# Kernel tuning notes

Measured on AMD Instinct MI355X. Metric: run time of the kernel, lower is better.

Reference implementation:

```python
import jax, jax.numpy as jnp
import numpy as np

D = 512; NH = 8; HD = D // NH; SR = 4; B = 8; HH = 64; WW = 64; N = HH * WW
Q = 200; C2 = D // 2; NH2 = NH // 2
SCALE = HD ** -0.5


def _ln(x, g, b):
    m = jnp.mean(x, -1, keepdims=True)
    v = jnp.mean((x - m) ** 2, -1, keepdims=True)
    return (x - m) * jax.lax.rsqrt(v + 1e-5) * g + b


def _relu6(x):
    return jnp.clip(x, 0.0, 6.0)


def _conv(x, w, b, s):
    y = jax.lax.conv_general_dilated(x, w, (s, s), 'VALID',
                                     dimension_numbers=('NCHW', 'OIHW', 'NCHW'))
    return y + b[None, :, None, None]


def _dwconv(x, w, b):
    y = jax.lax.conv_general_dilated(x, w, (1, 1), ((1, 1), (1, 1)),
                                     dimension_numbers=('NCHW', 'OIHW', 'NCHW'),
                                     feature_group_count=x.shape[1])
    return y + b[None, :, None, None]


def setup_inputs():
    key = jax.random.key(0)
    ks = jax.random.split(key, 16)
    conv4_std = float(np.sqrt(2.0 / (16 * D)))   # fan_out = 4*4*D
    conv2_std = float(np.sqrt(2.0 / (4 * D)))    # fan_out = 2*2*D
    dw_std = float(np.sqrt(2.0 / 9.0))           # fan_out = 3*3*C2/C2
    inp = {
        'query': jax.random.normal(ks[0], (Q, B, D), jnp.float32),
        'key': jax.random.normal(ks[1], (B, N, D), jnp.float32),
        'value': jax.random.normal(ks[2], (B, N, D), jnp.float32),
        'q_w': jax.random.normal(ks[3], (D, D), jnp.float32) * 0.02,
        'sr1_1_w': jax.random.normal(ks[4], (D, D, 4, 4), jnp.float32) * conv4_std,
        'sr1_1_b': jnp.zeros((D,), jnp.float32),
        'n1_1_g': jnp.ones((D,), jnp.float32),
        'n1_1_b': jnp.zeros((D,), jnp.float32),
        'sr1_2_w': jax.random.normal(ks[5], (D, D, 4, 4), jnp.float32) * conv4_std,
        'sr1_2_b': jnp.zeros((D,), jnp.float32),
        'n1_2_g': jnp.ones((D,), jnp.float32),
        'n1_2_b': jnp.zeros((D,), jnp.float32),
        'sr2_1_w': jax.random.normal(ks[6], (D, D, 2, 2), jnp.float32) * conv2_std,
        'sr2_1_b': jnp.zeros((D,), jnp.float32),
        'n2_1_g': jnp.ones((D,), jnp.float32),
        'n2_1_b': jnp.zeros((D,), jnp.float32),
        'sr2_2_w': jax.random.normal(ks[7], (D, D, 2, 2), jnp.float32) * conv2_std,
        'sr2_2_b': jnp.zeros((D,), jnp.float32),
        'n2_2_g': jnp.ones((D,), jnp.float32),
        'n2_2_b': jnp.zeros((D,), jnp.float32),
        'k1_w': jax.random.normal(ks[8], (C2, D), jnp.float32) * 0.02,
        'v1_w': jax.random.normal(ks[9], (C2, D), jnp.float32) * 0.02,
        'k2_w': jax.random.normal(ks[10], (C2, D), jnp.float32) * 0.02,
        'v2_w': jax.random.normal(ks[11], (C2, D), jnp.float32) * 0.02,
        'lc1_w': jax.random.normal(ks[12], (C2, 1, 3, 3), jnp.float32) * dw_std,
        'lc1_b': jnp.zeros((C2,), jnp.float32),
        'lc2_w': jax.random.normal(ks[13], (C2, 1, 3, 3), jnp.float32) * dw_std,
        'lc2_b': jnp.zeros((C2,), jnp.float32),
        'proj_w': jax.random.normal(ks[14], (D, D), jnp.float32) * 0.02,
        'proj_b': jnp.zeros((D,), jnp.float32),
        'H': HH,
        'W': WW,
    }
    return inp


def _forward(query, key, value, q_w,
             sr1_1_w, sr1_1_b, n1_1_g, n1_1_b, sr1_2_w, sr1_2_b, n1_2_g, n1_2_b,
             sr2_1_w, sr2_1_b, n2_1_g, n2_1_b, sr2_2_w, sr2_2_b, n2_2_g, n2_2_b,
             k1_w, v1_w, k2_w, v2_w, lc1_w, lc1_b, lc2_w, lc2_b,
             proj_w, proj_b, H, W):
    Qn, Bn, C = query.shape
    h1, w1 = H // SR, W // SR          # branch-1 reduced grid
    h2, w2 = H * 2 // SR, W * 2 // SR  # branch-2 reduced grid

    # q: note original does a raw reshape (Q,B,C)->(B,Q,nh,hd); replicate exactly
    q = (query @ q_w.T).reshape(Bn, Qn, NH, HD).transpose(0, 2, 1, 3)  # (B,NH,Q,HD)

    key_img = key.transpose(0, 2, 1).reshape(Bn, C, H, W)
    val_img = value.transpose(0, 2, 1).reshape(Bn, C, H, W)

    def reduce_branch(img, cw, cb, g, b, s):
        t = _conv(img, cw, cb, s).reshape(Bn, C, -1).transpose(0, 2, 1)  # (B,L,C)
        return _relu6(_ln(t, g, b))

    key_1 = reduce_branch(key_img, sr1_1_w, sr1_1_b, n1_1_g, n1_1_b, SR)
    val_1 = reduce_branch(val_img, sr1_2_w, sr1_2_b, n1_2_g, n1_2_b, SR)
    key_2 = reduce_branch(key_img, sr2_1_w, sr2_1_b, n2_1_g, n2_1_b, SR // 2)
    val_2 = reduce_branch(val_img, sr2_2_w, sr2_2_b, n2_2_g, n2_2_b, SR // 2)

    def heads(t, w):  # (B,L,C) -> (B,NH2,L,HD)
        return (t @ w.T).reshape(Bn, -1, NH2, HD).transpose(0, 2, 1, 3)

    k1 = heads(key_1, k1_w)
    v1 = heads(val_1, v1_w)
    k2 = heads(key_2, k2_w)
    v2 = heads(val_2, v2_w)

    def branch(qh, kh, vh, lw, lb, hh, ww):
        attn = jax.nn.softmax(jnp.einsum('bhqd,bhkd->bhqk', qh, kh) * SCALE, axis=-1)
        vimg = vh.transpose(0, 2, 1, 3).reshape(Bn, -1, C2).transpose(0, 2, 1)
        vimg = vimg.reshape(Bn, C2, hh, ww)
        vloc = _dwconv(vimg, lw, lb).reshape(Bn, NH2, HD, -1).transpose(0, 1, 3, 2)
        xh = jnp.einsum('bhqk,bhkd->bhqd', attn, vh + vloc)
        # original: .transpose(1,2).reshape(Q,B,C//2) -- raw reshape, replicate
        return xh.transpose(0, 2, 1, 3).reshape(Qn, Bn, C2)

    x1 = branch(q[:, :NH2], k1, v1, lc1_w, lc1_b, h1, w1)
    x2 = branch(q[:, NH2:], k2, v2, lc2_w, lc2_b, h2, w2)
    x = jnp.concatenate([x1, x2], axis=-1)
    return x @ proj_w.T + proj_b


def reference(query, key, value, q_w,
              sr1_1_w, sr1_1_b, n1_1_g, n1_1_b, sr1_2_w, sr1_2_b, n1_2_g, n1_2_b,
              sr2_1_w, sr2_1_b, n2_1_g, n2_1_b, sr2_2_w, sr2_2_b, n2_2_g, n2_2_b,
              k1_w, v1_w, k2_w, v2_w, lc1_w, lc1_b, lc2_w, lc2_b,
              proj_w, proj_b, H, W):
    return _forward(query, key, value, q_w,
                    sr1_1_w, sr1_1_b, n1_1_g, n1_1_b, sr1_2_w, sr1_2_b, n1_2_g, n1_2_b,
                    sr2_1_w, sr2_1_b, n2_1_g, n2_1_b, sr2_2_w, sr2_2_b, n2_2_g, n2_2_b,
                    k1_w, v1_w, k2_w, v2_w, lc1_w, lc1_b, lc2_w, lc2_b,
                    proj_w, proj_b, H, W)
```

## Files before the change

### kernel.cpp

```cpp
#include <hip/hip_runtime.h>
#include <cstddef>

#define QN   200
#define DIM  512
#define NHEAD 8
#define HD   64
#define C2   256
#define NH2  4
#define NTOK 4096

typedef unsigned short ushort_t;
typedef short s16x4 __attribute__((ext_vector_type(4)));
typedef short s16x8 __attribute__((ext_vector_type(8)));
typedef float f32x4 __attribute__((ext_vector_type(4)));

__device__ __forceinline__ unsigned short f2bf(float f) {
    unsigned int u = __float_as_uint(f);
    u += 0x7fffu + ((u >> 16) & 1u);
    return (unsigned short)(u >> 16);
}
__device__ __forceinline__ float bf2f(unsigned short u) {
    return __uint_as_float(((unsigned int)u) << 16);
}
__device__ __forceinline__ s16x8 pack8(float4 x, float4 y) {
    s16x8 v;
    v[0] = (short)f2bf(x.x); v[1] = (short)f2bf(x.y);
    v[2] = (short)f2bf(x.z); v[3] = (short)f2bf(x.w);
    v[4] = (short)f2bf(y.x); v[5] = (short)f2bf(y.y);
    v[6] = (short)f2bf(y.z); v[7] = (short)f2bf(y.w);
    return v;
}

__global__ __launch_bounds__(256) void cvt_f2b(
    const float* __restrict__ src, ushort_t* __restrict__ dst, int n8)
{
    const int i = blockIdx.x * 256 + threadIdx.x;
    if (i >= n8) return;
    const float4 a = ((const float4*)src)[i * 2];
    const float4 b = ((const float4*)src)[i * 2 + 1];
    ((s16x8*)dst)[i] = pack8(a, b);
}

struct CDesc { const float* s; ushort_t* d; };
struct CPack { CDesc c[7]; int bound[7]; };
__global__ __launch_bounds__(256) void prep_kernel(CPack pk)
{
    const int bid = blockIdx.x;
    int idx = 0;
#pragma unroll
    for (int i = 0; i < 6; ++i) idx += (bid >= pk.bound[i]);
    const int base = idx ? pk.bound[idx - 1] : 0;
    const int i = (bid - base) * 256 + threadIdx.x;
    const float4 a = ((const float4*)pk.c[idx].s)[i * 2];
    const float4 b = ((const float4*)pk.c[idx].s)[i * 2 + 1];
    ((s16x8*)pk.c[idx].d)[i] = pack8(a, b);
}

__global__ __launch_bounds__(256) void wtrans_kernel(
    const float* __restrict__ w, ushort_t* __restrict__ wt, int KK, int lKK)
{
    __shared__ float tile[512 * 17];
    const int c = blockIdx.x;
    const int K = KK << 9;
    const float* src = w + (size_t)c * K;
    ushort_t* dst = wt + (size_t)c * K;
    for (int i = threadIdx.x; i < K; i += 256) {
        int ci = i >> lKK, p = i & (KK - 1);
        tile[ci * (KK + 1) + p] = src[i];
    }
    __syncthreads();
    for (int i = threadIdx.x; i < K; i += 256) {
        int p = i >> 9, ci = i & 511;
        dst[i] = f2bf(tile[ci * (KK + 1) + p]);
    }
}

__global__ __launch_bounds__(256) void conv_gemm(
    const ushort_t* __restrict__ Ap, const ushort_t* __restrict__ Bp,
    float* __restrict__ Cp, int M, int N, int K, int klen,
    int lOW, int ls, int lMT)
{
    constexpr int ASZ = 128 * 64;
    constexpr int BSZ = 64 * 64;
    __shared__ short lds[2 * (ASZ + BSZ)];

    const int tid = threadIdx.x;
    const int bid = blockIdx.x;
    const int xcd = bid & 7;
    const int j = bid >> 3;
    const int nt = j & 7;
    const int mz = (j >> 3) * 8 + xcd;
    const int mt = mz & ((1 << lMT) - 1);
    const int z = mz >> lMT;
    const int m0 = mt * 128, n0 = nt * 64;
    const int kstart = z * klen;

    const int lane = tid & 63, wave = tid >> 6;
    const int l16 = lane & 15, quad = lane >> 4;
    const int wm = (wave >> 1) * 64;
    const int wn = (wave & 1) * 32;

    auto off = [](int r, int c) -> int {
        return (r << 6) + ((c ^ (r & 7)) << 3);
    };

    unsigned abase[4]; int offA[4], acx[4];
#pragma unroll
    for (int i = 0; i < 4; ++i) {
        const int g = tid + i * 256;
        const int r = g >> 3, c = g & 7;
        acx[i] = c * 8;
        offA[i] = off(r, c);
        const int OW = 1 << lOW;
        const int m = m0 + r;
        const int bidx = m >> (2 * lOW);
        const int pix = m & (OW * OW - 1);
        const int oy = pix >> lOW, ox = pix & (OW - 1);
        abase[i] = (unsigned)(bidx * NTOK + (oy << ls) * 64 + (ox << ls)) << 9;
    }
    unsigned bbase[2]; int offB[2], bcx[2];
#pragma unroll
    for (int i = 0; i < 2; ++i) {
        const int g = tid + i * 256;
        const int r = g >> 3, c = g & 7;
        bcx[i] = c * 8;
        offB[i] = off(r, c);
        bbase[i] = (unsigned)(n0 + r) * K;
    }

    s16x8 aR[4], bR[2];
    auto loadg = [&](int t) {
        const int k0 = kstart + t * 64;
#pragma unroll
        for (int i = 0; i < 4; ++i) {
            const int k = k0 + acx[i];
            const int p = k >> 9;
            const int ky = p >> ls, kx = p & ((1 << ls) - 1);
            const unsigned o = abase[i] + ((unsigned)(ky * 64 + kx) << 9) + (k & 511);
            aR[i] = *(const s16x8*)(Ap + o);
        }
#pragma unroll
        for (int i = 0; i < 2; ++i)
            bR[i] = *(const s16x8*)(Bp + bbase[i] + k0 + bcx[i]);
    };
    auto stg = [&](int buf) {
        short* A = lds + buf * (ASZ + BSZ);
        short* Bs = A + ASZ;
#pragma unroll
        for (int i = 0; i < 4; ++i) *(s16x8*)&A[offA[i]] = aR[i];
#pragma unroll
        for (int i = 0; i < 2; ++i) *(s16x8*)&Bs[offB[i]] = bR[i];
    };

    f32x4 acc[4][2];
#pragma unroll
    for (int a = 0; a < 4; ++a)
#pragma unroll
        for (int b = 0; b < 2; ++b)
            acc[a][b] = (f32x4){0.f, 0.f, 0.f, 0.f};

    loadg(0);
    stg(0);
    __syncthreads();
    const int nk = klen >> 6;
    for (int t = 0; t < nk; ++t) {
        if (t + 1 < nk) loadg(t + 1);
        const short* A = lds + (t & 1) * (ASZ + BSZ);
        const short* Bs = A + ASZ;
#pragma unroll
        for (int kk = 0; kk < 2; ++kk) {
            s16x8 af[4], bf[2];
#pragma unroll
            for (int f = 0; f < 4; ++f)
                af[f] = *(const s16x8*)&A[off(wm + f * 16 + l16, quad + kk * 4)];
#pragma unroll
            for (int f = 0; f < 2; ++f)
                bf[f] = *(const s16x8*)&Bs[off(wn + f * 16 + l16, quad + kk * 4)];
#pragma unroll
            for (int a = 0; a < 4; ++a)
#pragma unroll
                for (int b = 0; b < 2; ++b)
                    acc[a][b] = __builtin_amdgcn_mfma_f32_16x16x32_bf16(
                        af[a], bf[b], acc[a][b], 0, 0, 0);
        }
        if (t + 1 < nk) {
            stg((t + 1) & 1);
            __syncthreads();
        }
    }

    const unsigned zoff = (unsigned)z * (unsigned)M * (unsigned)N;
#pragma unroll
    for (int a = 0; a < 4; ++a) {
        const int m = m0 + wm + a * 16 + quad * 4;
#pragma unroll
        for (int b = 0; b < 2; ++b) {
            const int n = n0 + wn + b * 16 + l16;
#pragma unroll
            for (int r = 0; r < 4; ++r)
                Cp[zoff + (unsigned)(m + r) * N + n] = acc[a][b][r];
        }
    }
}

template <int OBF>
__device__ __forceinline__ void gemm64_k512(
    short* lds, const ushort_t* __restrict__ Ab, const ushort_t* __restrict__ Bp,
    const float* __restrict__ bias, void* __restrict__ Cp_,
    int m0, int n0, int N, float oscale)
{
    const int tid = threadIdx.x;
    const int lane = tid & 63, wave = tid >> 6;
    const int l16 = lane & 15, quad = lane >> 4;
    const int wm = (wave >> 1) * 32;
    const int wn = (wave & 1) * 32;

    auto off = [](int r, int c) -> int {
        return ((r >> 1) << 6) + (((((r & 1) << 2) | c) ^ ((r >> 1) & 7)) << 3);
    };

    const int cs = (tid & 3) * 8;
    const int ofA = off(tid >> 2, tid & 3);
    const unsigned ab = (unsigned)(m0 + (tid >> 2)) * 512;
    const unsigned bb = (unsigned)(n0 + (tid >> 2)) * 512;

    s16x8 aR, bR;
    auto loadg = [&](int t) {
        aR = *(const s16x8*)(Ab + ab + t * 32 + cs);
        bR = *(const s16x8*)(Bp + bb + t * 32 + cs);
    };
    auto stg = [&](int buf) {
        short* A = lds + buf * 4096;
        short* Bs = A + 2048;
        *(s16x8*)&A[ofA] = aR;
        *(s16x8*)&Bs[ofA] = bR;
    };

    f32x4 acc[2][2];
#pragma unroll
    for (int a = 0; a < 2; ++a)
#pragma unroll
        for (int b = 0; b < 2; ++b)
            acc[a][b] = (f32x4){0.f, 0.f, 0.f, 0.f};

    loadg(0); stg(0); __syncthreads();
#pragma unroll 1
    for (int t = 0; t < 16; ++t) {
        if (t + 1 < 16) loadg(t + 1);
        const short* A = lds + (t & 1) * 4096;
        const short* Bs = A + 2048;
        s16x8 af[2], bfv[2];
#pragma unroll
        for (int f = 0; f < 2; ++f)
            af[f] = *(const s16x8*)&A[off(wm + f * 16 + l16, quad)];
#pragma unroll
        for (int f = 0; f < 2; ++f)
            bfv[f] = *(const s16x8*)&Bs[off(wn + f * 16 + l16, quad)];
#pragma unroll
        for (int a = 0; a < 2; ++a)
#pragma unroll
            for (int b = 0; b < 2; ++b)
                acc[a][b] = __builtin_amdgcn_mfma_f32_16x16x32_bf16(
                    af[a], bfv[b], acc[a][b], 0, 0, 0);
        if (t + 1 < 16) { stg((t + 1) & 1); __syncthreads(); }
    }

#pragma unroll
    for (int a = 0; a < 2; ++a) {
        const int m = m0 + wm + a * 16 + quad * 4;
#pragma unroll
        for (int b = 0; b < 2; ++b) {
            const int n = n0 + wn + b * 16 + l16;
            const float bv = bias ? bias[n] : 0.f;
#pragma unroll
            for (int r = 0; r < 4; ++r) {
                const float val = acc[a][b][r] * oscale + bv;
                if constexpr (OBF)
                    ((ushort_t*)Cp_)[(unsigned)(m + r) * N + n] = f2bf(val);
                else
                    ((float*)Cp_)[(unsigned)(m + r) * N + n] = val;
            }
        }
    }
}

struct PDesc { const ushort_t* A; const ushort_t* B; ushort_t* C; int lnT; float scale; };
struct PPack { PDesc d[5]; int bound[5]; };
__global__ __launch_bounds__(256) void proj_gemm(PPack pk)
{
    __shared__ short lds[8192];
    const int bid = blockIdx.x;
    int idx = 0;
#pragma unroll
    for (int i = 0; i < 4; ++i) idx += (bid >= pk.bound[i]);
    const PDesc d = pk.d[idx];
    const int base = idx ? pk.bound[idx - 1] : 0;
    const int loc = bid - base;
    const int nt = loc & ((1 << d.lnT) - 1);
    const int mt = loc >> d.lnT;
    gemm64_k512<1>(lds, d.A, d.B, nullptr, d.C, mt * 64, nt * 64, 64 << d.lnT, d.scale);
}

__global__ __launch_bounds__(256) void final_gemm(
    const ushort_t* __restrict__ A, const ushort_t* __restrict__ B,
    const float* __restrict__ bias, float* __restrict__ C)
{
    __shared__ short lds[8192];
    const int m0 = (blockIdx.x >> 3) * 64;
    const int n0 = (blockIdx.x & 7) * 64;
    gemm64_k512<0>(lds, A, B, bias, C, m0, n0, 512, 1.0f);
}

__global__ __launch_bounds__(256) void ln_relu6_kernel(
    ushort_t* __restrict__ dst, const float* __restrict__ src, unsigned pstride,
    int np, const float* __restrict__ cb, const float* __restrict__ g,
    const float* __restrict__ bta)
{
    const int row = blockIdx.x * 4 + (threadIdx.x >> 6);
    const int lane = threadIdx.x & 63;
    float v[8];
#pragma unroll
    for (int j = 0; j < 8; ++j) v[j] = cb[lane + 64 * j];
    const float* p = src + (size_t)row * DIM;
    for (int ip = 0; ip < np; ++ip) {
#pragma unroll
        for (int j = 0; j < 8; ++j) v[j] += p[lane + 64 * j];
        p += pstride;
    }
    float s1 = 0.f, s2 = 0.f;
#pragma unroll
    for (int j = 0; j < 8; ++j) { s1 += v[j]; s2 += v[j] * v[j]; }
#pragma unroll
    for (int off = 32; off; off >>= 1) {
        s1 += __shfl_xor(s1, off, 64);
        s2 += __shfl_xor(s2, off, 64);
    }
    const float mean = s1 * (1.0f / DIM);
    const float var = s2 * (1.0f / DIM) - mean * mean;
    const float rstd = rsqrtf(var + 1e-5f);
    ushort_t* q = dst + (size_t)row * DIM;
#pragma unroll
    for (int j = 0; j < 8; ++j) {
        const int c = lane + 64 * j;
        float y = (v[j] - mean) * rstd * g[c] + bta[c];
        q[c] = f2bf(fminf(fmaxf(y, 0.0f), 6.0f));
    }
}

__device__ __forceinline__ void vplus_body(
    const ushort_t* __restrict__ vbuf, const float* __restrict__ lw,
    const float* __restrict__ lb, ushort_t* __restrict__ out,
    int lOW, int lL, int blk)
{
    const int idx = blk * 256 + threadIdx.x;
    const int c = idx & 255;
    const int pix = (idx >> 8) & ((1 << lL) - 1);
    const int b = idx >> (8 + lL);
    const int OW = 1 << lOW;
    const int y = pix >> lOW, x = pix & (OW - 1);
    float acc = lb[c];
#pragma unroll
    for (int dy = -1; dy <= 1; ++dy) {
        const int ny = y + dy;
        if ((unsigned)ny >= (unsigned)OW) continue;
#pragma unroll
        for (int dx = -1; dx <= 1; ++dx) {
            const int nx = x + dx;
            if ((unsigned)nx >= (unsigned)OW) continue;
            acc += bf2f(vbuf[(((unsigned)(b << lL) + ny * OW + nx) << 8) + c]) *
                   lw[c * 9 + (dy + 1) * 3 + (dx + 1)];
        }
    }
    out[idx] = f2bf(bf2f(vbuf[idx]) + acc);
}

__global__ __launch_bounds__(256) void vplus2_kernel(
    const ushort_t* v1, const float* w1, const float* b1, ushort_t* o1,
    const ushort_t* v2, const float* w2, const float* b2, ushort_t* o2)
{
    const int bid = blockIdx.x;
    if (bid < 2048) vplus_body(v1, w1, b1, o1, 4, 8, bid);
    else            vplus_body(v2, w2, b2, o2, 5, 10, bid - 2048);
}

template <int L>
__global__ __launch_bounds__(256) void attn_mfma(
    const ushort_t* __restrict__ qbuf, const ushort_t* __restrict__ kbuf,
    const ushort_t* __restrict__ vbuf, ushort_t* __restrict__ xbuf,
    int hoff, int coff)
{
    constexpr int SP = L + 12;
    constexpr int NV = L / 64;
    __shared__ float S[16][SP];
    __shared__ float invs[16];
    __shared__ alignas(16) short Qs[16][72];
    __shared__ alignas(16) short KV[64][72];

    const int tid = threadIdx.x;
    const int qt = blockIdx.x;
    const int h = blockIdx.y;
    const int b = blockIdx.z;
    const int lane = tid & 63, wave = tid >> 6;
    const int l16 = lane & 15, quad = lane >> 4;

    {
        const int r = tid >> 4, d0 = (tid & 15) * 4;
        int qi = qt * 16 + r; if (qi > QN - 1) qi = QN - 1;
        *(s16x4*)&Qs[r][d0] = *(const s16x4*)(
            qbuf + ((unsigned)(b * QN + qi) * NHEAD + hoff + h) * HD + d0);
    }

    const int klr = tid >> 2, kd0 = (tid & 3) * 16;
    for (int l0 = 0; l0 < L; l0 += 64) {
        const unsigned src = (unsigned)(b * L + l0 + klr) * C2 + h * HD + kd0;
        const s16x8 x0 = *(const s16x8*)(kbuf + src);
        const s16x8 x1 = *(const s16x8*)(kbuf + src + 8);
        __syncthreads();
        *(s16x8*)&KV[klr][kd0] = x0;
        *(s16x8*)&KV[klr][kd0 + 8] = x1;
        __syncthreads();
        f32x4 sacc = (f32x4){0.f, 0.f, 0.f, 0.f};
#pragma unroll
        for (int c = 0; c < 2; ++c) {
            const s16x8 af = *(const s16x8*)&Qs[l16][c * 32 + quad * 8];
            const s16x8 bf = *(const s16x8*)&KV[wave * 16 + l16][c * 32 + quad * 8];
            sacc = __builtin_amdgcn_mfma_f32_16x16x32_bf16(af, bf, sacc, 0, 0, 0);
        }
        const int col = l0 + wave * 16 + l16;
#pragma unroll
        for (int r = 0; r < 4; ++r) S[quad * 4 + r][col] = sacc[r];
    }
    __syncthreads();

#pragma unroll
    for (int rr = 0; rr < 4; ++rr) {
        const int row = wave * 4 + rr;
        float v[NV];
#pragma unroll
        for (int k = 0; k < NV; ++k) v[k] = S[row][lane + 64 * k];
        float m = -1e30f;
#pragma unroll
        for (int k = 0; k < NV; ++k) m = fmaxf(m, v[k]);
#pragma unroll
        for (int off = 32; off; off >>= 1) m = fmaxf(m, __shfl_xor(m, off, 64));
        float s = 0.f;
#pragma unroll
        for (int k = 0; k < NV; ++k) {
            v[k] = __expf(v[k] - m);
            s += v[k];
        }
#pragma unroll
        for (int off = 32; off; off >>= 1) s += __shfl_xor(s, off, 64);
#pragma unroll
        for (int k = 0; k < NV; ++k) S[row][lane + 64 * k] = v[k];
        if (lane == 0) invs[row] = 1.0f / s;
    }

    f32x4 oacc = (f32x4){0.f, 0.f, 0.f, 0.f};
    const int vl = tid >> 4, vd0 = (tid & 15) * 4;
    for (int l0 = 0; l0 < L; l0 += 64) {
        s16x4 vr[4];
#pragma unroll
        for (int p = 0; p < 4; ++p)
            vr[p] = *(const s16x4*)(
                vbuf + (unsigned)(b * L + l0 + p * 16 + vl) * C2 + h * HD + vd0);
        __syncthreads();
#pragma unroll
        for (int p = 0; p < 4; ++p) {
            const int ll = p * 16 + vl;
            KV[vd0 + 0][ll] = vr[p][0];
            KV[vd0 + 1][ll] = vr[p][1];
            KV[vd0 + 2][ll] = vr[p][2];
            KV[vd0 + 3][ll] = vr[p][3];
        }
        __syncthreads();
#pragma unroll
        for (int c = 0; c < 2; ++c) {
            const float4 p0 = *(const float4*)&S[l16][l0 + c * 32 + quad * 8];
            const float4 p1 = *(const float4*)&S[l16][l0 + c * 32 + quad * 8 + 4];
            const s16x8 af = pack8(p0, p1);
            const s16x8 bf = *(const s16x8*)&KV[wave * 16 + l16][c * 32 + quad * 8];
            oacc = __builtin_amdgcn_mfma_f32_16x16x32_bf16(af, bf, oacc, 0, 0, 0);
        }
    }

    const int dcol = wave * 16 + l16;
#pragma unroll
    for (int r = 0; r < 4; ++r) {
        const int q = quad * 4 + r;
        const int qi = qt * 16 + q;
        if (qi < QN) {
            const float val = oacc[r] * invs[q];
            const int flat = ((b * QN + qi) * NH2 + h) * HD + dcol;
            xbuf[(unsigned)(flat >> 8) * DIM + coff + (flat & 255)] = f2bf(val);
        }
    }
}

extern "C" void kernel_launch(void* const* d_in, const int* in_sizes, int n_in,
                              void* d_out, int out_size, void* d_ws, size_t ws_size,
                              hipStream_t stream)
{
    const float* query   = (const float*)d_in[0];
    const float* key     = (const float*)d_in[1];
    const float* value   = (const float*)d_in[2];
    const float* q_w     = (const float*)d_in[3];
    const float* sr1_1_w = (const float*)d_in[4];
    const float* sr1_1_b = (const float*)d_in[5];
    const float* n1_1_g  = (const float*)d_in[6];
    const float* n1_1_b  = (const float*)d_in[7];
    const float* sr1_2_w = (const float*)d_in[8];
    const float* sr1_2_b = (const float*)d_in[9];
    const float* n1_2_g  = (const float*)d_in[10];
    const float* n1_2_b  = (const float*)d_in[11];
    const float* sr2_1_w = (const float*)d_in[12];
    const float* sr2_1_b = (const float*)d_in[13];
    const float* n2_1_g  = (const float*)d_in[14];
    const float* n2_1_b  = (const float*)d_in[15];
    const float* sr2_2_w = (const float*)d_in[16];
    const float* sr2_2_b = (const float*)d_in[17];
    const float* n2_2_g  = (const float*)d_in[18];
    const float* n2_2_b  = (const float*)d_in[19];
    const float* k1_w    = (const float*)d_in[20];
    const float* v1_w    = (const float*)d_in[21];
    const float* k2_w    = (const float*)d_in[22];
    const float* v2_w    = (const float*)d_in[23];
    const float* lc1_w   = (const float*)d_in[24];
    const float* lc1_b   = (const float*)d_in[25];
    const float* lc2_w   = (const float*)d_in[26];
    const float* lc2_b   = (const float*)d_in[27];
    const float* proj_w  = (const float*)d_in[28];
    const float* proj_b  = (const float*)d_in[29];
    float* out = (float*)d_out;
    char* ws = (char*)d_ws;

    ushort_t* IMGB = (ushort_t*)(ws + 0);
    float*    SCR  = (float*)(ws + 33554432);
    ushort_t* WT1  = (ushort_t*)(ws + 50331648);
    ushort_t* KEY1 = (ushort_t*)(ws + 58720256);
    ushort_t* VAL1 = (ushort_t*)(ws + 60817408);
    ushort_t* KEY2 = (ushort_t*)(ws + 62914560);
    ushort_t* VAL2 = (ushort_t*)(ws + 71303168);
    ushort_t* WT2  = (ushort_t*)d_out;
    ushort_t* QRYB = (ushort_t*)(ws + 0);
    ushort_t* WQ   = (ushort_t*)(ws + 1638400);
    ushort_t* WK1  = (ushort_t*)(ws + 2162688);
    ushort_t* WV1  = (ushort_t*)(ws + 2424832);
    ushort_t* WK2  = (ushort_t*)(ws + 2686976);
    ushort_t* WV2  = (ushort_t*)(ws + 2949120);
    ushort_t* WP   = (ushort_t*)(ws + 3211264);
    ushort_t* QBUF = (ushort_t*)(ws + 3735552);
    ushort_t* XBUF = (ushort_t*)(ws + 5373952);
    ushort_t* K1   = (ushort_t*)(ws + 7012352);
    ushort_t* V1   = (ushort_t*)(ws + 8060928);
    ushort_t* VP1  = (ushort_t*)(ws + 9109504);
    ushort_t* K2   = (ushort_t*)(ws + 10158080);
    ushort_t* V2   = (ushort_t*)(ws + 14352384);
    ushort_t* VP2  = (ushort_t*)(ws + 18546688);

    cvt_f2b<<<8192, 256, 0, stream>>>(key, IMGB, 2097152);
    wtrans_kernel<<<512, 256, 0, stream>>>(sr1_1_w, WT1, 16, 4);
    conv_gemm<<<512, 256, 0, stream>>>(IMGB, WT1, SCR, 2048, 512, 8192, 2048, 4, 2, 4);
    ln_relu6_kernel<<<512, 256, 0, stream>>>(KEY1, SCR, 1048576u, 4, sr1_1_b, n1_1_g, n1_1_b);
    wtrans_kernel<<<512, 256, 0, stream>>>(sr2_1_w, WT2, 4, 2);
    conv_gemm<<<512, 256, 0, stream>>>(IMGB, WT2, SCR, 8192, 512, 2048, 2048, 5, 1, 6);
    ln_relu6_kernel<<<2048, 256, 0, stream>>>(KEY2, SCR, 0u, 1, sr2_1_b, n2_1_g, n2_1_b);

    cvt_f2b<<<8192, 256, 0, stream>>>(value, IMGB, 2097152);
    wtrans_kernel<<<512, 256, 0, stream>>>(sr1_2_w, WT1, 16, 4);
    conv_gemm<<<512, 256, 0, stream>>>(IMGB, WT1, SCR, 2048, 512, 8192, 2048, 4, 2, 4);
    ln_relu6_kernel<<<512, 256, 0, stream>>>(VAL1, SCR, 1048576u, 4, sr1_2_b, n1_2_g, n1_2_b);
    wtrans_kernel<<<512, 256, 0, stream>>>(sr2_2_w, WT2, 4, 2);
    conv_gemm<<<512, 256, 0, stream>>>(IMGB, WT2, SCR, 8192, 512, 2048, 2048, 5, 1, 6);
    ln_relu6_kernel<<<2048, 256, 0, stream>>>(VAL2, SCR, 0u, 1, sr2_2_b, n2_2_g, n2_2_b);

    CPack cp;
    cp.c[0] = {query,  QRYB}; cp.c[1] = {q_w, WQ};  cp.c[2] = {k1_w, WK1};
    cp.c[3] = {v1_w,   WV1};  cp.c[4] = {k2_w, WK2}; cp.c[5] = {v2_w, WV2};
    cp.c[6] = {proj_w, WP};
    cp.bound[0] = 400; cp.bound[1] = 528; cp.bound[2] = 592; cp.bound[3] = 656;
    cp.bound[4] = 720; cp.bound[5] = 784; cp.bound[6] = 912;
    prep_kernel<<<912, 256, 0, stream>>>(cp);

    PPack pp;
    pp.d[0] = {QRYB, WQ,  QBUF, 3, 0.125f};
    pp.d[1] = {KEY1, WK1, K1,   2, 1.0f};
    pp.d[2] = {VAL1, WV1, V1,   2, 1.0f};
    pp.d[3] = {KEY2, WK2, K2,   2, 1.0f};
    pp.d[4] = {VAL2, WV2, V2,   2, 1.0f};
    pp.bound[0] = 200; pp.bound[1] = 328; pp.bound[2] = 456; pp.bound[3] = 968;
    pp.bound[4] = 1480;
    proj_gemm<<<1480, 256, 0, stream>>>(pp);

    vplus2_kernel<<<10240, 256, 0, stream>>>(V1, lc1_w, lc1_b, VP1,
                                             V2, lc2_w, lc2_b, VP2);

    attn_mfma<256><<<dim3(13, 4, 8), 256, 0, stream>>>(QBUF, K1, VP1, XBUF, 0, 0);
    attn_mfma<1024><<<dim3(13, 4, 8), 256, 0, stream>>>(QBUF, K2, VP2, XBUF, 4, 256);

    final_gemm<<<200, 256, 0, stream>>>(XBUF, WP, proj_b, out);
}
```

Measured before the change: 479.6 us.

## Batch key/value conv branches into joint launches with direct-to-LDS loads

Key and value conversion, weight transposes, conv GEMMs and LayerNorms are merged into single launches covering both streams, giving separate workspace buffers for each. The conv GEMM tile grows to 128x128, loads go straight into LDS through global_load_lds, and it drops from double buffering to one buffer with two barriers per step. Split-K now uses twice as many splits, so the LN reduction sums more partials. The aims are to cut launch count, raise occupancy and move data more efficiently, at the cost of losing load/compute overlap and using a larger workspace.

```diff
diff --git a/kernel.cpp b/kernel.cpp
--- a/kernel.cpp
+++ b/kernel.cpp
@@ -1,5 +1,6 @@
 #include <hip/hip_runtime.h>
 #include <cstddef>
+#include <cstdint>
 
 #define QN   200
 #define DIM  512
@@ -10,6 +11,7 @@
 #define NTOK 4096
 
 typedef unsigned short ushort_t;
+typedef unsigned int u32;
 typedef short s16x4 __attribute__((ext_vector_type(4)));
 typedef short s16x8 __attribute__((ext_vector_type(8)));
 typedef float f32x4 __attribute__((ext_vector_type(4)));
@@ -31,24 +33,20 @@
     return v;
 }
 
-__global__ __launch_bounds__(256) void cvt_f2b(
-    const float* __restrict__ src, ushort_t* __restrict__ dst, int n8)
-{
-    const int i = blockIdx.x * 256 + threadIdx.x;
-    if (i >= n8) return;
-    const float4 a = ((const float4*)src)[i * 2];
-    const float4 b = ((const float4*)src)[i * 2 + 1];
-    ((s16x8*)dst)[i] = pack8(a, b);
+__device__ __forceinline__ void gld16(const ushort_t* g, short* l) {
+    __builtin_amdgcn_global_load_lds(
+        (const __attribute__((address_space(1))) u32*)g,
+        (__attribute__((address_space(3))) u32*)l, 16, 0, 0);
 }
 
 struct CDesc { const float* s; ushort_t* d; };
-struct CPack { CDesc c[7]; int bound[7]; };
-__global__ __launch_bounds__(256) void prep_kernel(CPack pk)
+struct CPack { CDesc c[9]; int bound[9]; };
+__global__ __launch_bounds__(256) void cvt_all(CPack pk)
 {
     const int bid = blockIdx.x;
     int idx = 0;
 #pragma unroll
-    for (int i = 0; i < 6; ++i) idx += (bid >= pk.bound[i]);
+    for (int i = 0; i < 8; ++i) idx += (bid >= pk.bound[i]);
     const int base = idx ? pk.bound[idx - 1] : 0;
     const int i = (bid - base) * 256 + threadIdx.x;
     const float4 a = ((const float4*)pk.c[idx].s)[i * 2];
@@ -56,14 +54,17 @@
     ((s16x8*)pk.c[idx].d)[i] = pack8(a, b);
 }
 
-__global__ __launch_bounds__(256) void wtrans_kernel(
-    const float* __restrict__ w, ushort_t* __restrict__ wt, int KK, int lKK)
+struct WDesc { const float* s; ushort_t* d; int KK; int lKK; };
+struct WPack { WDesc w[4]; };
+__global__ __launch_bounds__(256) void wtrans4(WPack pk)
 {
     __shared__ float tile[512 * 17];
-    const int c = blockIdx.x;
+    const WDesc d = pk.w[blockIdx.x >> 9];
+    const int c = blockIdx.x & 511;
+    const int KK = d.KK, lKK = d.lKK;
     const int K = KK << 9;
-    const float* src = w + (size_t)c * K;
-    ushort_t* dst = wt + (size_t)c * K;
+    const float* src = d.s + (size_t)c * K;
+    ushort_t* dst = d.d + (size_t)c * K;
     for (int i = threadIdx.x; i < K; i += 256) {
         int ci = i >> lKK, p = i & (KK - 1);
         tile[ci * (KK + 1) + p] = src[i];
@@ -76,129 +77,107 @@
 }
 
 __global__ __launch_bounds__(256) void conv_gemm(
-    const ushort_t* __restrict__ Ap, const ushort_t* __restrict__ Bp,
-    float* __restrict__ Cp, int M, int N, int K, int klen,
-    int lOW, int ls, int lMT)
-{
-    constexpr int ASZ = 128 * 64;
-    constexpr int BSZ = 64 * 64;
-    __shared__ short lds[2 * (ASZ + BSZ)];
+    const ushort_t* __restrict__ ApK, const ushort_t* __restrict__ BpK,
+    float* __restrict__ CpK,
+    const ushort_t* __restrict__ ApV, const ushort_t* __restrict__ BpV,
+    float* __restrict__ CpV,
+    int M, int K, int klen, int lOW, int ls, int lMT)
+{
+    __shared__ short lds[16384];
 
     const int tid = threadIdx.x;
-    const int bid = blockIdx.x;
+    int bid = blockIdx.x;
+    const ushort_t* Ap; const ushort_t* Bp; float* Cp;
+    if (bid < 512) { Ap = ApK; Bp = BpK; Cp = CpK; }
+    else           { Ap = ApV; Bp = BpV; Cp = CpV; bid -= 512; }
+
     const int xcd = bid & 7;
     const int j = bid >> 3;
-    const int nt = j & 7;
-    const int mz = (j >> 3) * 8 + xcd;
+    const int nt = j & 3;
+    const int mz = (j >> 2) * 8 + xcd;
     const int mt = mz & ((1 << lMT) - 1);
     const int z = mz >> lMT;
-    const int m0 = mt * 128, n0 = nt * 64;
+    const int m0 = mt * 128, n0 = nt * 128;
     const int kstart = z * klen;
 
     const int lane = tid & 63, wave = tid >> 6;
     const int l16 = lane & 15, quad = lane >> 4;
     const int wm = (wave >> 1) * 64;
-    const int wn = (wave & 1) * 32;
-
-    auto off = [](int r, int c) -> int {
-        return (r << 6) + ((c ^ (r & 7)) << 3);
-    };
-
-    unsigned abase[4]; int offA[4], acx[4];
+    const int wn = (wave & 1) * 64;
+
+    unsigned abase[4]; int acb[4];
+    const ushort_t* bptr[4];
+    short* ldsA[4]; short* ldsB[4];
+    const int OW = 1 << lOW;
 #pragma unroll
     for (int i = 0; i < 4; ++i) {
-        const int g = tid + i * 256;
+        const int g = i * 256 + tid;
         const int r = g >> 3, c = g & 7;
-        acx[i] = c * 8;
-        offA[i] = off(r, c);
-        const int OW = 1 << lOW;
+        acb[i] = ((c ^ (r & 7)) << 3);
         const int m = m0 + r;
         const int bidx = m >> (2 * lOW);
         const int pix = m & (OW * OW - 1);
         const int oy = pix >> lOW, ox = pix & (OW - 1);
         abase[i] = (unsigned)(bidx * NTOK + (oy << ls) * 64 + (ox << ls)) << 9;
-    }
-    unsigned bbase[2]; int offB[2], bcx[2];
-#pragma unroll
-    for (int i = 0; i < 2; ++i) {
-        const int g = tid + i * 256;
-        const int r = g >> 3, c = g & 7;
-        bcx[i] = c * 8;
-        offB[i] = off(r, c);
-        bbase[i] = (unsigned)(n0 + r) * K;
-    }
-
-    s16x8 aR[4], bR[2];
-    auto loadg = [&](int t) {
-        const int k0 = kstart + t * 64;
+        bptr[i] = Bp + (unsigned)(n0 + r) * K + kstart + acb[i];
+        ldsA[i] = lds + (i * 256 + wave * 64) * 8;
+        ldsB[i] = lds + 8192 + (i * 256 + wave * 64) * 8;
+    }
+
+    f32x4 acc[4][4];
+#pragma unroll
+    for (int a = 0; a < 4; ++a)
+#pragma unroll
+        for (int b = 0; b < 4; ++b)
+            acc[a][b] = (f32x4){0.f, 0.f, 0.f, 0.f};
+
+    const int lsm = (1 << ls) - 1;
+    const int nk = klen >> 6;
+#pragma unroll 1
+    for (int t = 0; t < nk; ++t) {
+        const int k0 = kstart + (t << 6);
 #pragma unroll
         for (int i = 0; i < 4; ++i) {
-            const int k = k0 + acx[i];
+            const int k = k0 + acb[i];
             const int p = k >> 9;
-            const int ky = p >> ls, kx = p & ((1 << ls) - 1);
-            const unsigned o = abase[i] + ((unsigned)(ky * 64 + kx) << 9) + (k & 511);
-            aR[i] = *(const s16x8*)(Ap + o);
-        }
-#pragma unroll
-        for (int i = 0; i < 2; ++i)
-            bR[i] = *(const s16x8*)(Bp + bbase[i] + k0 + bcx[i]);
-    };
-    auto stg = [&](int buf) {
-        short* A = lds + buf * (ASZ + BSZ);
-        short* Bs = A + ASZ;
-#pragma unroll
-        for (int i = 0; i < 4; ++i) *(s16x8*)&A[offA[i]] = aR[i];
-#pragma unroll
-        for (int i = 0; i < 2; ++i) *(s16x8*)&Bs[offB[i]] = bR[i];
-    };
-
-    f32x4 acc[4][2];
-#pragma unroll
-    for (int a = 0; a < 4; ++a)
-#pragma unroll
-        for (int b = 0; b < 2; ++b)
-            acc[a][b] = (f32x4){0.f, 0.f, 0.f, 0.f};
-
-    loadg(0);
-    stg(0);
-    __syncthreads();
-    const int nk = klen >> 6;
-    for (int t = 0; t < nk; ++t) {
-        if (t + 1 < nk) loadg(t + 1);
-        const short* A = lds + (t & 1) * (ASZ + BSZ);
-        const short* Bs = A + ASZ;
+            const int ky = p >> ls, kx = p & lsm;
+            gld16(Ap + abase[i] + ((unsigned)(ky * 64 + kx) << 9) + (k & 511), ldsA[i]);
+        }
+#pragma unroll
+        for (int i = 0; i < 4; ++i)
+            gld16(bptr[i] + (t << 6), ldsB[i]);
+        __syncthreads();
+
 #pragma unroll
         for (int kk = 0; kk < 2; ++kk) {
-            s16x8 af[4], bf[2];
+            const int sw = ((quad + kk * 4) ^ (l16 & 7)) << 3;
+            s16x8 af[4], bfv[4];
 #pragma unroll
             for (int f = 0; f < 4; ++f)
-                af[f] = *(const s16x8*)&A[off(wm + f * 16 + l16, quad + kk * 4)];
-#pragma unroll
-            for (int f = 0; f < 2; ++f)
-                bf[f] = *(const s16x8*)&Bs[off(wn + f * 16 + l16, quad + kk * 4)];
+                af[f] = *(const s16x8*)&lds[(wm + f * 16 + l16) * 64 + sw];
+#pragma unroll
+            for (int f = 0; f < 4; ++f)
+                bfv[f] = *(const s16x8*)&lds[8192 + (wn + f * 16 + l16) * 64 + sw];
 #pragma unroll
             for (int a = 0; a < 4; ++a)
 #pragma unroll
-                for (int b = 0; b < 2; ++b)
+                for (int b = 0; b < 4; ++b)
                     acc[a][b] = __builtin_amdgcn_mfma_f32_16x16x32_bf16(
-                        af[a], bf[b], acc[a][b], 0, 0, 0);
-        }
-        if (t + 1 < nk) {
-            stg((t + 1) & 1);
-            __syncthreads();
-        }
-    }
-
-    const unsigned zoff = (unsigned)z * (unsigned)M * (unsigned)N;
+                        af[a], bfv[b], acc[a][b], 0, 0, 0);
+        }
+        __syncthreads();
+    }
+
+    float* __restrict__ Cz = Cp + (size_t)z * M * 512;
 #pragma unroll
     for (int a = 0; a < 4; ++a) {
         const int m = m0 + wm + a * 16 + quad * 4;
 #pragma unroll
-        for (int b = 0; b < 2; ++b) {
+        for (int b = 0; b < 4; ++b) {
             const int n = n0 + wn + b * 16 + l16;
 #pragma unroll
             for (int r = 0; r < 4; ++r)
-                Cp[zoff + (unsigned)(m + r) * N + n] = acc[a][b][r];
+                Cz[(unsigned)(m + r) * 512 + n] = acc[a][b][r];
         }
     }
 }
@@ -311,12 +290,20 @@
     gemm64_k512<0>(lds, A, B, bias, C, m0, n0, 512, 1.0f);
 }
 
-__global__ __launch_bounds__(256) void ln_relu6_kernel(
-    ushort_t* __restrict__ dst, const float* __restrict__ src, unsigned pstride,
-    int np, const float* __restrict__ cb, const float* __restrict__ g,
-    const float* __restrict__ bta)
-{
-    const int row = blockIdx.x * 4 + (threadIdx.x >> 6);
+__global__ __launch_bounds__(256) void ln2_kernel(
+    ushort_t* __restrict__ d1, const float* __restrict__ s1,
+    const float* __restrict__ cb1, const float* __restrict__ g1,
+    const float* __restrict__ b1,
+    ushort_t* __restrict__ d2, const float* __restrict__ s2,
+    const float* __restrict__ cb2, const float* __restrict__ g2,
+    const float* __restrict__ b2,
+    unsigned pstride, int np, int half)
+{
+    ushort_t* dst; const float* src; const float* cb; const float* g; const float* bta;
+    int blk = blockIdx.x;
+    if (blk < half) { dst = d1; src = s1; cb = cb1; g = g1; bta = b1; }
+    else            { dst = d2; src = s2; cb = cb2; g = g2; bta = b2; blk -= half; }
+    const int row = blk * 4 + (threadIdx.x >> 6);
     const int lane = threadIdx.x & 63;
     float v[8];
 #pragma unroll
@@ -327,16 +314,16 @@
         for (int j = 0; j < 8; ++j) v[j] += p[lane + 64 * j];
         p += pstride;
     }
-    float s1 = 0.f, s2 = 0.f;
-#pragma unroll
-    for (int j = 0; j < 8; ++j) { s1 += v[j]; s2 += v[j] * v[j]; }
+    float s1v = 0.f, s2v = 0.f;
+#pragma unroll
+    for (int j = 0; j < 8; ++j) { s1v += v[j]; s2v += v[j] * v[j]; }
 #pragma unroll
     for (int off = 32; off; off >>= 1) {
-        s1 += __shfl_xor(s1, off, 64);
-        s2 += __shfl_xor(s2, off, 64);
-    }
-    const float mean = s1 * (1.0f / DIM);
-    const float var = s2 * (1.0f / DIM) - mean * mean;
+        s1v += __shfl_xor(s1v, off, 64);
+        s2v += __shfl_xor(s2v, off, 64);
+    }
+    const float mean = s1v * (1.0f / DIM);
+    const float var = s2v * (1.0f / DIM) - mean * mean;
     const float rstd = rsqrtf(var + 1e-5f);
     ushort_t* q = dst + (size_t)row * DIM;
 #pragma unroll
@@ -534,53 +521,59 @@
     float* out = (float*)d_out;
     char* ws = (char*)d_ws;
 
-    ushort_t* IMGB = (ushort_t*)(ws + 0);
-    float*    SCR  = (float*)(ws + 33554432);
-    ushort_t* WT1  = (ushort_t*)(ws + 50331648);
-    ushort_t* KEY1 = (ushort_t*)(ws + 58720256);
-    ushort_t* VAL1 = (ushort_t*)(ws + 60817408);
-    ushort_t* KEY2 = (ushort_t*)(ws + 62914560);
-    ushort_t* VAL2 = (ushort_t*)(ws + 71303168);
-    ushort_t* WT2  = (ushort_t*)d_out;
-    ushort_t* QRYB = (ushort_t*)(ws + 0);
-    ushort_t* WQ   = (ushort_t*)(ws + 1638400);
-    ushort_t* WK1  = (ushort_t*)(ws + 2162688);
-    ushort_t* WV1  = (ushort_t*)(ws + 2424832);
-    ushort_t* WK2  = (ushort_t*)(ws + 2686976);
-    ushort_t* WV2  = (ushort_t*)(ws + 2949120);
-    ushort_t* WP   = (ushort_t*)(ws + 3211264);
-    ushort_t* QBUF = (ushort_t*)(ws + 3735552);
-    ushort_t* XBUF = (ushort_t*)(ws + 5373952);
-    ushort_t* K1   = (ushort_t*)(ws + 7012352);
-    ushort_t* V1   = (ushort_t*)(ws + 8060928);
-    ushort_t* VP1  = (ushort_t*)(ws + 9109504);
-    ushort_t* K2   = (ushort_t*)(ws + 10158080);
-    ushort_t* V2   = (ushort_t*)(ws + 14352384);
-    ushort_t* VP2  = (ushort_t*)(ws + 18546688);
-
-    cvt_f2b<<<8192, 256, 0, stream>>>(key, IMGB, 2097152);
-    wtrans_kernel<<<512, 256, 0, stream>>>(sr1_1_w, WT1, 16, 4);
-    conv_gemm<<<512, 256, 0, stream>>>(IMGB, WT1, SCR, 2048, 512, 8192, 2048, 4, 2, 4);
-    ln_relu6_kernel<<<512, 256, 0, stream>>>(KEY1, SCR, 1048576u, 4, sr1_1_b, n1_1_g, n1_1_b);
-    wtrans_kernel<<<512, 256, 0, stream>>>(sr2_1_w, WT2, 4, 2);
-    conv_gemm<<<512, 256, 0, stream>>>(IMGB, WT2, SCR, 8192, 512, 2048, 2048, 5, 1, 6);
-    ln_relu6_kernel<<<2048, 256, 0, stream>>>(KEY2, SCR, 0u, 1, sr2_1_b, n2_1_g, n2_1_b);
-
-    cvt_f2b<<<8192, 256, 0, stream>>>(value, IMGB, 2097152);
-    wtrans_kernel<<<512, 256, 0, stream>>>(sr1_2_w, WT1, 16, 4);
-    conv_gemm<<<512, 256, 0, stream>>>(IMGB, WT1, SCR, 2048, 512, 8192, 2048, 4, 2, 4);
-    ln_relu6_kernel<<<512, 256, 0, stream>>>(VAL1, SCR, 1048576u, 4, sr1_2_b, n1_2_g, n1_2_b);
-    wtrans_kernel<<<512, 256, 0, stream>>>(sr2_2_w, WT2, 4, 2);
-    conv_gemm<<<512, 256, 0, stream>>>(IMGB, WT2, SCR, 8192, 512, 2048, 2048, 5, 1, 6);
-    ln_relu6_kernel<<<2048, 256, 0, stream>>>(VAL2, SCR, 0u, 1, sr2_2_b, n2_2_g, n2_2_b);
+    ushort_t* IMGK = (ushort_t*)(ws + 0);
+    ushort_t* IMGV = (ushort_t*)(ws + 33554432);
+    float*    SCRK = (float*)(ws + 67108864);
+    float*    SCRV = (float*)(ws + 100663296);
+    ushort_t* WT1K = (ushort_t*)(ws + 134217728);
+    ushort_t* WT1V = (ushort_t*)(ws + 142606336);
+    ushort_t* WT2K = (ushort_t*)(ws + 150994944);
+    ushort_t* WT2V = (ushort_t*)(ws + 153092096);
+    ushort_t* KEY1 = (ushort_t*)(ws + 155189248);
+    ushort_t* VAL1 = (ushort_t*)(ws + 157286400);
+    ushort_t* KEY2 = (ushort_t*)(ws + 159383552);
+    ushort_t* VAL2 = (ushort_t*)(ws + 167772160);
+    ushort_t* QRYB = (ushort_t*)(ws + 176160768);
+    ushort_t* WQ   = (ushort_t*)(ws + 177799168);
+    ushort_t* WK1  = (ushort_t*)(ws + 178323456);
+    ushort_t* WV1  = (ushort_t*)(ws + 178585600);
+    ushort_t* WK2  = (ushort_t*)(ws + 178847744);
+    ushort_t* WV2  = (ushort_t*)(ws + 179109888);
+    ushort_t* WP   = (ushort_t*)(ws + 179372032);
+    ushort_t* QBUF = (ushort_t*)(ws + 179896320);
+    ushort_t* XBUF = (ushort_t*)(ws + 181534720);
+    ushort_t* K1   = (ushort_t*)(ws + 183173120);
+    ushort_t* V1   = (ushort_t*)(ws + 184221696);
+    ushort_t* VP1  = (ushort_t*)(ws + 185270272);
+    ushort_t* K2   = (ushort_t*)(ws + 186318848);
+    ushort_t* V2   = (ushort_t*)(ws + 190513152);
+    ushort_t* VP2  = (ushort_t*)(ws + 194707456);
 
     CPack cp;
-    cp.c[0] = {query,  QRYB}; cp.c[1] = {q_w, WQ};  cp.c[2] = {k1_w, WK1};
-    cp.c[3] = {v1_w,   WV1};  cp.c[4] = {k2_w, WK2}; cp.c[5] = {v2_w, WV2};
-    cp.c[6] = {proj_w, WP};
-    cp.bound[0] = 400; cp.bound[1] = 528; cp.bound[2] = 592; cp.bound[3] = 656;
-    cp.bound[4] = 720; cp.bound[5] = 784; cp.bound[6] = 912;
-    prep_kernel<<<912, 256, 0, stream>>>(cp);
+    cp.c[0] = {key,   IMGK}; cp.c[1] = {value, IMGV}; cp.c[2] = {query, QRYB};
+    cp.c[3] = {q_w,   WQ};   cp.c[4] = {k1_w,  WK1};  cp.c[5] = {v1_w,  WV1};
+    cp.c[6] = {k2_w,  WK2};  cp.c[7] = {v2_w,  WV2};  cp.c[8] = {proj_w, WP};
+    cp.bound[0] = 8192;  cp.bound[1] = 16384; cp.bound[2] = 16784;
+    cp.bound[3] = 16912; cp.bound[4] = 16976; cp.bound[5] = 17040;
+    cp.bound[6] = 17104; cp.bound[7] = 17168; cp.bound[8] = 17296;
+    cvt_all<<<17296, 256, 0, stream>>>(cp);
+
+    WPack wp;
+    wp.w[0] = {sr1_1_w, WT1K, 16, 4}; wp.w[1] = {sr1_2_w, WT1V, 16, 4};
+    wp.w[2] = {sr2_1_w, WT2K, 4, 2};  wp.w[3] = {sr2_2_w, WT2V, 4, 2};
+    wtrans4<<<2048, 256, 0, stream>>>(wp);
+
+    conv_gemm<<<1024, 256, 0, stream>>>(IMGK, WT1K, SCRK, IMGV, WT1V, SCRV,
+                                        2048, 8192, 1024, 4, 2, 4);
+    ln2_kernel<<<1024, 256, 0, stream>>>(KEY1, SCRK, sr1_1_b, n1_1_g, n1_1_b,
+                                         VAL1, SCRV, sr1_2_b, n1_2_g, n1_2_b,
+                                         1048576u, 8, 512);
+
+    conv_gemm<<<1024, 256, 0, stream>>>(IMGK, WT2K, SCRK, IMGV, WT2V, SCRV,
+                                        8192, 2048, 1024, 5, 1, 6);
+    ln2_kernel<<<4096, 256, 0, stream>>>(KEY2, SCRK, sr2_1_b, n2_1_g, n2_1_b,
+                                         VAL2, SCRV, sr2_2_b, n2_2_g, n2_2_b,
+                                         4194304u, 2, 2048);
 
     PPack pp;
     pp.d[0] = {QRYB, WQ,  QBUF, 3, 0.125f};
```

After: 466.9 us. 1.03x faster.
